# Kernel tuning notes

Hardware: AMD Instinct MI355X
Metric: run time of the kernel (lower is better)

The kernel has to match this reference:

```python
import jax, jax.numpy as jnp
import numpy as np

N_HEAD = 16
LORA_DIM = 16
LORA_ALPHA = 32


def setup_inputs() -> dict:
    key = jax.random.key(0)
    ks = jax.random.split(key, 8)
    B, S, D = 2, 2048, 1024
    std = 0.02
    return {
        "x": jax.random.normal(ks[0], (B, S, D), jnp.float32),
        "c_attn_w": jax.random.normal(ks[1], (D, 3 * D), jnp.float32) * std,
        "c_attn_b": jnp.zeros((3 * D,), jnp.float32),
        "c_proj_w": jax.random.normal(ks[2], (D, D), jnp.float32) * std,
        "c_proj_b": jnp.zeros((D,), jnp.float32),
        "q_a1": jax.random.normal(ks[3], (D, LORA_DIM), jnp.float32) * std,
        "q_a2": jax.random.normal(ks[4], (LORA_DIM, D), jnp.float32) * std,
        "v_a1": jax.random.normal(ks[5], (D, LORA_DIM), jnp.float32) * std,
        "v_a2": jax.random.normal(ks[6], (LORA_DIM, D), jnp.float32) * std,
    }


def reference(x, c_attn_w, c_attn_b, c_proj_w, c_proj_b, q_a1, q_a2, v_a1, v_a2):
    B, S, D = x.shape
    H = N_HEAD
    hd = D // H
    # NOTE: original code uses adapter_dim / adapter_alpha as the scale
    lora_scale = jnp.float32(LORA_DIM / LORA_ALPHA)

    qkv = x @ c_attn_w + c_attn_b                      # [B,S,3D]
    q, k, v = jnp.split(qkv, 3, axis=-1)
    q = q + ((x @ q_a1) @ q_a2) * lora_scale
    v = v + ((x @ v_a1) @ v_a2) * lora_scale

    def heads(t):
        return t.reshape(B, S, H, hd).transpose(0, 2, 1, 3)  # [B,H,S,hd]

    qh, kh, vh = heads(q), heads(k), heads(v)

    w = jnp.einsum('bhqd,bhkd->bhqk', qh, kh) / jnp.sqrt(jnp.float32(hd))
    bias = jnp.tril(jnp.ones((S, S), dtype=w.dtype))   # causal mask
    w = w * bias - jnp.float32(1e10) * (1 - bias)
    w = jax.nn.softmax(w, axis=-1)
    a = jnp.einsum('bhqk,bhkd->bhqd', w, vh)
    a = a.transpose(0, 2, 1, 3).reshape(B, S, D)       # merge heads
    a = a @ c_proj_w + c_proj_b

    present = jnp.stack((kh, vh))                      # [2,B,H,S,hd]
    return a, present
```

## Files before the change

kernel.cpp:

```cpp
#include <hip/hip_runtime.h>

#define T_TOK 4096
#define D_DIM 1024
#define N3    3072
#define S_LEN 2048
#define NH    16
#define HD    64
#define KAUG  1056

#define OUT_A_ELEMS   4194304
#define OUT_KV_ELEMS  4194304

typedef __attribute__((ext_vector_type(4))) float f32x4;
typedef __attribute__((ext_vector_type(16))) float f32x16;
typedef _Float16 f16x8 __attribute__((ext_vector_type(8)));
typedef _Float16 f16x4 __attribute__((ext_vector_type(4)));

union U4h { unsigned u[4]; f16x8 v; };

#define GHASH(r) ((((r) >> 1) ^ ((r) >> 3)) & 3)

__device__ __forceinline__ unsigned cvtpkh(float a, float b) {
    unsigned r;
    asm("v_cvt_pkrtz_f16_f32 %0, %1, %2" : "=v"(r) : "v"(a), "v"(b));
    return r;
}

#define GLL16(gp, lp) __builtin_amdgcn_global_load_lds( \
    (const __attribute__((address_space(1))) unsigned int*)(gp), \
    (__attribute__((address_space(3))) unsigned int*)(lp), 16, 0, 0)

#define MFMA16F(A, B, C) __builtin_amdgcn_mfma_f32_16x16x32_f16(A, B, C, 0, 0, 0)
#define MFMA32F(A, B, C) __builtin_amdgcn_mfma_f32_32x32x16_f16(A, B, C, 0, 0, 0)

__global__ __launch_bounds__(256) void lora1_v2(const float* __restrict__ x,
    const float* __restrict__ qa1, const float* __restrict__ va1,
    float* __restrict__ tq, float* __restrict__ tv) {
    int tid = threadIdx.x;
    int w = tid >> 6;
    int lane = tid & 63;
    int t = blockIdx.x * 4 + w;
    int cg = lane & 7;
    int ks = lane >> 3;
    const float* a1 = (cg < 4) ? qa1 : va1;
    int c4 = (cg & 3) * 4;
    const float* xr = x + (size_t)t * D_DIM + ks * 128;
    const float* ar = a1 + (size_t)(ks * 128) * 16 + c4;
    float4 acc = make_float4(0.f, 0.f, 0.f, 0.f);
#pragma unroll 8
    for (int j = 0; j < 128; ++j) {
        float xv = xr[j];
        float4 av = *(const float4*)&ar[j * 16];
        acc.x = fmaf(xv, av.x, acc.x);
        acc.y = fmaf(xv, av.y, acc.y);
        acc.z = fmaf(xv, av.z, acc.z);
        acc.w = fmaf(xv, av.w, acc.w);
    }
#pragma unroll
    for (int m = 8; m < 64; m <<= 1) {
        acc.x += __shfl_xor(acc.x, m);
        acc.y += __shfl_xor(acc.y, m);
        acc.z += __shfl_xor(acc.z, m);
        acc.w += __shfl_xor(acc.w, m);
    }
    if (lane < 8) {
        float* dst = (cg < 4) ? &tq[t * 16 + c4] : &tv[t * 16 + (cg - 4) * 4];
        *(float4*)dst = acc;
    }
}

__global__ __launch_bounds__(256) void splitA_f16(const float* __restrict__ x,
    const float* __restrict__ tq, const float* __restrict__ tv,
    _Float16* __restrict__ af) {
    int idx = blockIdx.x * 256 + threadIdx.x;
    const int total = T_TOK * (KAUG / 4);
    if (idx >= total) return;
    int t = idx / (KAUG / 4);
    int c4 = (idx - t * (KAUG / 4)) * 4;
    float4 v;
    if (c4 < D_DIM)           v = *(const float4*)&x[(size_t)t * D_DIM + c4];
    else if (c4 < D_DIM + 16) v = *(const float4*)&tq[t * 16 + (c4 - D_DIM)];
    else                      v = *(const float4*)&tv[t * 16 + (c4 - D_DIM - 16)];
    f16x4 h;
    h[0] = (_Float16)v.x; h[1] = (_Float16)v.y;
    h[2] = (_Float16)v.z; h[3] = (_Float16)v.w;
    *(f16x4*)&af[(size_t)t * KAUG + c4] = h;
}

__global__ __launch_bounds__(256) void splitW_f16(const float* __restrict__ w,
    const float* __restrict__ qa2, const float* __restrict__ va2,
    _Float16* __restrict__ bf) {
    __shared__ float T[32][65];
    int bn = blockIdx.x;
    int bk = blockIdx.y;
    int tid = threadIdx.x;
#pragma unroll
    for (int u = 0; u < 2; ++u) {
        int id = tid + 256 * u;
        int kr = id >> 4;
        int n4 = (id & 15) * 4;
        int k = bk * 32 + kr;
        int n = bn * 64 + n4;
        float4 v = make_float4(0.f, 0.f, 0.f, 0.f);
        if (k < D_DIM) {
            v = *(const float4*)&w[(size_t)k * N3 + n];
        } else if (k < D_DIM + 16) {
            if (n < D_DIM) {
                float4 q4 = *(const float4*)&qa2[(k - D_DIM) * D_DIM + n];
                v = make_float4(q4.x * 0.5f, q4.y * 0.5f, q4.z * 0.5f, q4.w * 0.5f);
            }
        } else {
            if (n >= 2 * D_DIM) {
                float4 q4 = *(const float4*)&va2[(k - D_DIM - 16) * D_DIM + (n - 2 * D_DIM)];
                v = make_float4(q4.x * 0.5f, q4.y * 0.5f, q4.z * 0.5f, q4.w * 0.5f);
            }
        }
        T[kr][n4 + 0] = v.x; T[kr][n4 + 1] = v.y;
        T[kr][n4 + 2] = v.z; T[kr][n4 + 3] = v.w;
    }
    __syncthreads();
    int n = tid >> 2;
    int k8 = (tid & 3) * 8;
    f16x8 hv;
#pragma unroll
    for (int j = 0; j < 8; ++j) hv[j] = (_Float16)T[k8 + j][n];
    int nr = bn * 64 + n;
    int gsw = (tid & 3) ^ GHASH(nr);
    size_t ro = (size_t)nr * KAUG + bk * 32 + gsw * 8;
    *(f16x8*)&bf[ro] = hv;
}

__global__ __launch_bounds__(256) void wprep_f16(const float* __restrict__ w,
    _Float16* __restrict__ bf) {
    __shared__ float T[32][65];
    int bn = blockIdx.x;
    int bk = blockIdx.y;
    int tid = threadIdx.x;
#pragma unroll
    for (int u = 0; u < 2; ++u) {
        int id = tid + 256 * u;
        int kr = id >> 4;
        int n4 = (id & 15) * 4;
        float4 v = *(const float4*)&w[(size_t)(bk * 32 + kr) * D_DIM + bn * 64 + n4];
        T[kr][n4 + 0] = v.x; T[kr][n4 + 1] = v.y;
        T[kr][n4 + 2] = v.z; T[kr][n4 + 3] = v.w;
    }
    __syncthreads();
    int n = tid >> 2;
    int k8 = (tid & 3) * 8;
    f16x8 hv;
#pragma unroll
    for (int j = 0; j < 8; ++j) hv[j] = (_Float16)T[k8 + j][n];
    int nr = bn * 64 + n;
    int gsw = (tid & 3) ^ GHASH(nr);
    size_t ro = (size_t)nr * D_DIM + bk * 32 + gsw * 8;
    *(f16x8*)&bf[ro] = hv;
}

__global__ __launch_bounds__(256, 3) void qkv_mfma(
    const _Float16* __restrict__ a_g, const _Float16* __restrict__ b_g,
    const float* __restrict__ bias, int mode,
    float* __restrict__ qstage, float* __restrict__ pres,
    _Float16* __restrict__ qf16, _Float16* __restrict__ kp,
    _Float16* __restrict__ vt) {
    __shared__ _Float16 Bf[2][2][128 * 32];
    int id = blockIdx.y * 24 + blockIdx.x;
    int nid = (id & 7) * 96 + (id >> 3);
    int bn = nid % 24;
    int bm = nid / 24;
    int tid = threadIdx.x;
    int w = tid >> 6, l = tid & 63;
    int wr = w >> 1, wc = w & 1;

    f32x4 acc[4][4];
#pragma unroll
    for (int i = 0; i < 4; ++i)
#pragma unroll
        for (int j = 0; j < 4; ++j)
            acc[i][j] = (f32x4){0.f, 0.f, 0.f, 0.f};

    int srow = l >> 2;
    int sk = (l & 3) * 8;
    const size_t b_base0 = (size_t)(bn * 128 + w * 32 + srow) * KAUG + sk;
    const size_t b_base1 = b_base0 + (size_t)16 * KAUG;
    const int ldso0 = (w * 32) * 32;
    const int ldso1 = (w * 32 + 16) * 32;

    int lrow = l & 15;
    int lg = l >> 4;

    const _Float16* aF[4];
#pragma unroll
    for (int i = 0; i < 4; ++i) {
        int row = bm * 128 + wr * 64 + i * 16 + lrow;
        aF[i] = a_g + (size_t)row * KAUG + lg * 8;
    }
    int roB[4];
#pragma unroll
    for (int j = 0; j < 4; ++j) {
        int Rb = wc * 64 + j * 16 + lrow;
        roB[j] = Rb * 32 + ((lg ^ GHASH(Rb)) * 8);
    }

    f16x8 cA0[4], cA1[4], nA0[4], nA1[4];

    GLL16(b_g + b_base0,      &Bf[0][0][ldso0]);
    GLL16(b_g + b_base1,      &Bf[0][0][ldso1]);
    GLL16(b_g + b_base0 + 32, &Bf[0][1][ldso0]);
    GLL16(b_g + b_base1 + 32, &Bf[0][1][ldso1]);
#pragma unroll
    for (int i = 0; i < 4; ++i) {
        cA0[i] = *(const f16x8*)(aF[i]);
        cA1[i] = *(const f16x8*)(aF[i] + 32);
    }
    asm volatile("s_waitcnt vmcnt(0)" ::: "memory");
    __builtin_amdgcn_s_barrier();

    for (int r = 0; r < 17; ++r) {
        int cur = r & 1;
        if (r < 16) {
            int kn = (r + 1) * 64;
            GLL16(b_g + b_base0 + kn, &Bf[cur ^ 1][0][ldso0]);
            GLL16(b_g + b_base1 + kn, &Bf[cur ^ 1][0][ldso1]);
            if (r < 15) {
                GLL16(b_g + b_base0 + kn + 32, &Bf[cur ^ 1][1][ldso0]);
                GLL16(b_g + b_base1 + kn + 32, &Bf[cur ^ 1][1][ldso1]);
            }
            __builtin_amdgcn_sched_barrier(0);
#pragma unroll
            for (int i = 0; i < 4; ++i) nA0[i] = *(const f16x8*)(aF[i] + kn);
            if (r < 15) {
#pragma unroll
                for (int i = 0; i < 4; ++i) nA1[i] = *(const f16x8*)(aF[i] + kn + 32);
            }
        }
        f16x8 fb[4];
#pragma unroll
        for (int j = 0; j < 4; ++j) fb[j] = *(const f16x8*)&Bf[cur][0][roB[j]];
#pragma unroll
        for (int i = 0; i < 4; ++i)
#pragma unroll
            for (int j = 0; j < 4; ++j)
                acc[i][j] = MFMA16F(cA0[i], fb[j], acc[i][j]);
        if (r < 16) {
#pragma unroll
            for (int j = 0; j < 4; ++j) fb[j] = *(const f16x8*)&Bf[cur][1][roB[j]];
#pragma unroll
            for (int i = 0; i < 4; ++i)
#pragma unroll
                for (int j = 0; j < 4; ++j)
                    acc[i][j] = MFMA16F(cA1[i], fb[j], acc[i][j]);
            if (r < 15) asm volatile("s_waitcnt vmcnt(8)" ::: "memory");
            else        asm volatile("s_waitcnt vmcnt(4)" ::: "memory");
            __builtin_amdgcn_s_barrier();
#pragma unroll
            for (int i = 0; i < 4; ++i) cA0[i] = nA0[i];
            if (r < 15) {
#pragma unroll
                for (int i = 0; i < 4; ++i) cA1[i] = nA1[i];
            }
        }
    }

    int seg = bn >> 3;
    int bb = bm >> 4;
#pragma unroll
    for (int j = 0; j < 4; ++j) {
        int n = bn * 128 + wc * 64 + j * 16 + lrow;
        float bz = bias[n];
        int h = (n >> 6) & 15;
        int d = n & 63;
        size_t rowbase = (size_t)(bb * NH + h) * S_LEN;
#pragma unroll
        for (int i = 0; i < 4; ++i) {
            int tb = bm * 128 + wr * 64 + i * 16 + (l >> 4) * 4;
            int s0 = tb & 2047;
            if (seg == 0) {
                if (mode == 0) {
#pragma unroll
                    for (int r = 0; r < 4; ++r)
                        qf16[(rowbase + s0 + r) * HD + d] =
                            (_Float16)((acc[i][j][r] + bz) * 0.125f);
                } else {
#pragma unroll
                    for (int r = 0; r < 4; ++r)
                        qstage[(rowbase + s0 + r) * HD + d] =
                            (acc[i][j][r] + bz) * 0.125f;
                }
            } else if (seg == 1) {
                int gsw = d >> 3;
#pragma unroll
                for (int r = 0; r < 4; ++r) {
                    float v = acc[i][j][r] + bz;
                    int s = s0 + r;
                    pres[(rowbase + s) * HD + d] = v;
                    if (mode == 0)
                        kp[(rowbase + s) * HD + ((gsw ^ (s & 7)) << 3) + (d & 7)] =
                            (_Float16)v;
                }
            } else {
                f16x4 pk;
#pragma unroll
                for (int r = 0; r < 4; ++r) {
                    float v = acc[i][j][r] + bz;
                    pres[OUT_KV_ELEMS + (rowbase + s0 + r) * HD + d] = v;
                    pk[r] = (_Float16)v;
                }
                if (mode == 0) {
                    int gp = ((s0 >> 3) & 7) ^ (d & 7);
                    *(f16x4*)&vt[((size_t)(bb * NH + h) * 64 + d) * 2048
                                 + (s0 & ~63) + (gp << 3) + (s0 & 7)] = pk;
                }
            }
        }
    }
}

__global__ __launch_bounds__(256, 3) void proj_mfma(
    const _Float16* __restrict__ a_g, const _Float16* __restrict__ b_g,
    const float* __restrict__ bias, float* __restrict__ outp) {
    __shared__ _Float16 Bf[2][2][128 * 32];
    int id = blockIdx.y * 8 + blockIdx.x;
    int nid = (id & 7) * 32 + (id >> 3);
    int bn = nid % 8;
    int bm = nid / 8;
    int tid = threadIdx.x;
    int w = tid >> 6, l = tid & 63;
    int wr = w >> 1, wc = w & 1;

    f32x4 acc[4][4];
#pragma unroll
    for (int i = 0; i < 4; ++i)
#pragma unroll
        for (int j = 0; j < 4; ++j)
            acc[i][j] = (f32x4){0.f, 0.f, 0.f, 0.f};

    int srow = l >> 2;
    int sk = (l & 3) * 8;
    const size_t b_base0 = (size_t)(bn * 128 + w * 32 + srow) * D_DIM + sk;
    const size_t b_base1 = b_base0 + (size_t)16 * D_DIM;
    const int ldso0 = (w * 32) * 32;
    const int ldso1 = (w * 32 + 16) * 32;

    int lrow = l & 15;
    int lg = l >> 4;

    const _Float16* aF[4];
#pragma unroll
    for (int i = 0; i < 4; ++i) {
        int row = bm * 128 + wr * 64 + i * 16 + lrow;
        aF[i] = a_g + (size_t)row * D_DIM + lg * 8;
    }
    int roB[4];
#pragma unroll
    for (int j = 0; j < 4; ++j) {
        int Rb = wc * 64 + j * 16 + lrow;
        roB[j] = Rb * 32 + ((lg ^ GHASH(Rb)) * 8);
    }

    f16x8 cA0[4], cA1[4], nA0[4], nA1[4];

    GLL16(b_g + b_base0,      &Bf[0][0][ldso0]);
    GLL16(b_g + b_base1,      &Bf[0][0][ldso1]);
    GLL16(b_g + b_base0 + 32, &Bf[0][1][ldso0]);
    GLL16(b_g + b_base1 + 32, &Bf[0][1][ldso1]);
#pragma unroll
    for (int i = 0; i < 4; ++i) {
        cA0[i] = *(const f16x8*)(aF[i]);
        cA1[i] = *(const f16x8*)(aF[i] + 32);
    }
    asm volatile("s_waitcnt vmcnt(0)" ::: "memory");
    __builtin_amdgcn_s_barrier();

    for (int r = 0; r < 16; ++r) {
        int cur = r & 1;
        if (r < 15) {
            int kn = (r + 1) * 64;
            GLL16(b_g + b_base0 + kn,      &Bf[cur ^ 1][0][ldso0]);
            GLL16(b_g + b_base1 + kn,      &Bf[cur ^ 1][0][ldso1]);
            GLL16(b_g + b_base0 + kn + 32, &Bf[cur ^ 1][1][ldso0]);
            GLL16(b_g + b_base1 + kn + 32, &Bf[cur ^ 1][1][ldso1]);
            __builtin_amdgcn_sched_barrier(0);
#pragma unroll
            for (int i = 0; i < 4; ++i) {
                nA0[i] = *(const f16x8*)(aF[i] + kn);
                nA1[i] = *(const f16x8*)(aF[i] + kn + 32);
            }
        }
        f16x8 fb[4];
#pragma unroll
        for (int j = 0; j < 4; ++j) fb[j] = *(const f16x8*)&Bf[cur][0][roB[j]];
#pragma unroll
        for (int i = 0; i < 4; ++i)
#pragma unroll
            for (int j = 0; j < 4; ++j)
                acc[i][j] = MFMA16F(cA0[i], fb[j], acc[i][j]);
#pragma unroll
        for (int j = 0; j < 4; ++j) fb[j] = *(const f16x8*)&Bf[cur][1][roB[j]];
#pragma unroll
        for (int i = 0; i < 4; ++i)
#pragma unroll
            for (int j = 0; j < 4; ++j)
                acc[i][j] = MFMA16F(cA1[i], fb[j], acc[i][j]);
        if (r < 15) {
            asm volatile("s_waitcnt vmcnt(8)" ::: "memory");
            __builtin_amdgcn_s_barrier();
#pragma unroll
            for (int i = 0; i < 4; ++i) { cA0[i] = nA0[i]; cA1[i] = nA1[i]; }
        }
    }

#pragma unroll
    for (int j = 0; j < 4; ++j) {
        int n = bn * 128 + wc * 64 + j * 16 + lrow;
        float bz = bias[n];
#pragma unroll
        for (int i = 0; i < 4; ++i) {
            int tbase = bm * 128 + wr * 64 + i * 16 + (l >> 4) * 4;
#pragma unroll
            for (int r = 0; r < 4; ++r)
                outp[(size_t)(tbase + r) * D_DIM + n] = acc[i][j][r] + bz;
        }
    }
}

__device__ __forceinline__ void stage_tile(
    const _Float16* __restrict__ kp, const _Float16* __restrict__ vt,
    _Float16 (*ldsb)[4096], int w, int l, int bh, int kv0) {
    if (w < 2) {
        const _Float16* gp = kp
            + ((size_t)bh * 2048 + kv0 + w * 32 + (l >> 3)) * 64 + (l & 7) * 8;
        _Float16* lp = ldsb[0] + (w * 32) * 64;
#pragma unroll
        for (int i = 0; i < 4; ++i)
            GLL16(gp + i * 512, lp + i * 512);
    } else {
        int wv = w - 2;
        const _Float16* gp = vt
            + ((size_t)bh * 64 + wv * 32 + (l >> 3)) * 2048 + kv0 + (l & 7) * 8;
        _Float16* lp = ldsb[1] + (wv * 32) * 64;
#pragma unroll
        for (int i = 0; i < 4; ++i)
            GLL16(gp + (size_t)i * 8 * 2048, lp + i * 512);
    }
}

#define QROW(r) ((((r) & 3) + 8 * ((r) >> 2)) + 4 * g)

__global__ __launch_bounds__(256, 4) void attn_mfma(
    const _Float16* __restrict__ q_h,
    const _Float16* __restrict__ kp, const _Float16* __restrict__ vt,
    _Float16* __restrict__ aout) {
    __shared__ __align__(16) _Float16 lds[2][2][4096];
    int bh = blockIdx.x;
    int qi = (int)gridDim.y - 1 - blockIdx.y;
    int tid = threadIdx.x;
    int w = tid >> 6, l = tid & 63;
    int qloc = l & 31, g = l >> 5;
    int q0 = qi * 128;
    int qg = q0 + w * 32 + qloc;

    f16x8 qf[4];
    {
        const _Float16* qrow = q_h + ((size_t)bh * S_LEN + qg) * HD;
#pragma unroll
        for (int t = 0; t < 4; ++t)
            qf[t] = *(const f16x8*)&qrow[t * 16 + g * 8];
    }

    f32x16 o0, o1;
#pragma unroll
    for (int r = 0; r < 16; ++r) { o0[r] = 0.f; o1[r] = 0.f; }
    float m_run = -1e30f, l_run = 0.f;

    int nt = 2 * qi + 2;
    int qwmax = q0 + w * 32 + 31;

    stage_tile(kp, vt, lds[0], w, l, bh, 0);
    __syncthreads();

    for (int t = 0; t < nt; ++t) {
        int kv0 = t * 64;
        int bi = t & 1;
        if (t + 1 < nt)
            stage_tile(kp, vt, lds[bi ^ 1], w, l, bh, (t + 1) * 64);

        if (kv0 <= qwmax) {
            const _Float16* Kp = lds[bi][0];
            const _Float16* Vp = lds[bi][1];

            f32x16 s0, s1;
#pragma unroll
            for (int r = 0; r < 16; ++r) { s0[r] = 0.f; s1[r] = 0.f; }

            __builtin_amdgcn_s_setprio(1);
#pragma unroll
            for (int tt = 0; tt < 4; ++tt) {
                int gr = ((2 * tt + g) ^ (qloc & 7)) * 8;
                f16x8 a0 = *(const f16x8*)&Kp[qloc * 64 + gr];
                f16x8 a1 = *(const f16x8*)&Kp[(32 + qloc) * 64 + gr];
                s0 = MFMA32F(a0, qf[tt], s0);
                s1 = MFMA32F(a1, qf[tt], s1);
            }
            __builtin_amdgcn_s_setprio(0);

            if (kv0 + 63 > q0 + w * 32) {
#pragma unroll
                for (int r = 0; r < 16; ++r) {
                    int kk = kv0 + QROW(r);
                    if (kk > qg)      s0[r] = -1e30f;
                    if (kk + 32 > qg) s1[r] = -1e30f;
                }
            }

            float mx = s0[0];
#pragma unroll
            for (int r = 1; r < 16; ++r) mx = fmaxf(mx, s0[r]);
#pragma unroll
            for (int r = 0; r < 16; ++r) mx = fmaxf(mx, s1[r]);
            mx = fmaxf(mx, __shfl_xor(mx, 32));
            float mnew = fmaxf(m_run, mx);
            float al = __expf(m_run - mnew);
            m_run = mnew;
            float rs = 0.f;
#pragma unroll
            for (int r = 0; r < 16; ++r) { s0[r] = __expf(s0[r] - mnew); rs += s0[r]; }
#pragma unroll
            for (int r = 0; r < 16; ++r) { s1[r] = __expf(s1[r] - mnew); rs += s1[r]; }
            rs += __shfl_xor(rs, 32);
            l_run = l_run * al + rs;
#pragma unroll
            for (int r = 0; r < 16; ++r) {
                float ar = __shfl(al, QROW(r));
                o0[r] *= ar; o1[r] *= ar;
            }

            __builtin_amdgcn_s_setprio(1);
#pragma unroll
            for (int ks = 0; ks < 4; ++ks) {
                const int b = (ks & 1) * 8;
                unsigned w0, w1, w2, w3;
                if (ks < 2) {
                    w0 = cvtpkh(s0[b + 0], s0[b + 1]);
                    w1 = cvtpkh(s0[b + 2], s0[b + 3]);
                    w2 = cvtpkh(s0[b + 4], s0[b + 5]);
                    w3 = cvtpkh(s0[b + 6], s0[b + 7]);
                } else {
                    w0 = cvtpkh(s1[b + 0], s1[b + 1]);
                    w1 = cvtpkh(s1[b + 2], s1[b + 3]);
                    w2 = cvtpkh(s1[b + 4], s1[b + 5]);
                    w3 = cvtpkh(s1[b + 6], s1[b + 7]);
                }
                asm("v_permlane32_swap_b32 %0, %1" : "+v"(w0), "+v"(w2));
                asm("v_permlane32_swap_b32 %0, %1" : "+v"(w1), "+v"(w3));
                U4h u; u.u[0] = w0; u.u[1] = w1; u.u[2] = w2; u.u[3] = w3;
                f16x8 pa = u.v;
                int gr = ((2 * ks + g) ^ (qloc & 7)) * 8;
                f16x8 v0 = *(const f16x8*)&Vp[qloc * 64 + gr];
                f16x8 v1 = *(const f16x8*)&Vp[(32 + qloc) * 64 + gr];
                o0 = MFMA32F(pa, v0, o0);
                o1 = MFMA32F(pa, v1, o1);
            }
            __builtin_amdgcn_s_setprio(0);
        }
        __syncthreads();
    }

    int bb = bh >> 4, h = bh & 15;
#pragma unroll
    for (int r = 0; r < 16; ++r) {
        float li = __shfl(l_run, QROW(r));
        float inv = 1.f / li;
        int qq = q0 + w * 32 + QROW(r);
        size_t base = ((size_t)(bb * S_LEN + qq)) * D_DIM + h * HD + qloc;
        aout[base]      = (_Float16)(o0[r] * inv);
        aout[base + 32] = (_Float16)(o1[r] * inv);
    }
}

#define LSTR 68
__global__ __launch_bounds__(256) void attn_kernel(const float* __restrict__ q_s,
    const float* __restrict__ k_s, const float* __restrict__ v_s,
    float* __restrict__ a_s) {
    __shared__ float Qt[64][LSTR];
    __shared__ float KP[64][LSTR];
    __shared__ float Vs[64][LSTR];
    int bh = blockIdx.x;
    int qi = 31 - blockIdx.y;
    int tid = threadIdx.x;
    int tx = tid & 15, ty = tid >> 4;

#pragma unroll
    for (int qq = 0; qq < 4; ++qq) {
        int q  = qq * 16 + (tid >> 4);
        int d4 = (tid & 15) * 4;
        float4 v = *(const float4*)&q_s[((size_t)bh * S_LEN + qi * 64 + q) * HD + d4];
        Qt[d4 + 0][q] = v.x; Qt[d4 + 1][q] = v.y;
        Qt[d4 + 2][q] = v.z; Qt[d4 + 3][q] = v.w;
    }

    float o[4][4];
#pragma unroll
    for (int r = 0; r < 4; ++r)
#pragma unroll
        for (int c = 0; c < 4; ++c) o[r][c] = 0.f;
    float mrow[4] = {-1e30f, -1e30f, -1e30f, -1e30f};
    float lrow[4] = {0.f, 0.f, 0.f, 0.f};

    for (int kt = 0; kt <= qi; ++kt) {
        __syncthreads();
#pragma unroll
        for (int kk2 = 0; kk2 < 4; ++kk2) {
            int k  = kk2 * 16 + (tid >> 4);
            int d4 = (tid & 15) * 4;
            size_t rowoff = ((size_t)bh * S_LEN + kt * 64 + k) * HD + d4;
            float4 kv4 = *(const float4*)&k_s[rowoff];
            KP[d4 + 0][k] = kv4.x; KP[d4 + 1][k] = kv4.y;
            KP[d4 + 2][k] = kv4.z; KP[d4 + 3][k] = kv4.w;
            float4 vv4 = *(const float4*)&v_s[rowoff];
            *(float4*)&Vs[k][d4] = vv4;
        }
        __syncthreads();

        float s[4][4];
#pragma unroll
        for (int r = 0; r < 4; ++r)
#pragma unroll
            for (int c = 0; c < 4; ++c) s[r][c] = 0.f;
#pragma unroll 8
        for (int d = 0; d < 64; ++d) {
            float4 qv = *(const float4*)&Qt[d][ty * 4];
            float4 kv = *(const float4*)&KP[d][tx * 4];
            float qa[4] = {qv.x, qv.y, qv.z, qv.w};
            float ka[4] = {kv.x, kv.y, kv.z, kv.w};
#pragma unroll
            for (int r = 0; r < 4; ++r)
#pragma unroll
                for (int c = 0; c < 4; ++c)
                    s[r][c] = fmaf(qa[r], ka[c], s[r][c]);
        }
        if (kt == qi) {
#pragma unroll
            for (int r = 0; r < 4; ++r)
#pragma unroll
                for (int c = 0; c < 4; ++c)
                    if (tx * 4 + c > ty * 4 + r) s[r][c] = -1e30f;
        }
        __syncthreads();

        float p[4][4];
#pragma unroll
        for (int r = 0; r < 4; ++r) {
            float mx = fmaxf(fmaxf(s[r][0], s[r][1]), fmaxf(s[r][2], s[r][3]));
            mx = fmaxf(mx, __shfl_xor(mx, 1));
            mx = fmaxf(mx, __shfl_xor(mx, 2));
            mx = fmaxf(mx, __shfl_xor(mx, 4));
            mx = fmaxf(mx, __shfl_xor(mx, 8));
            float mn = fmaxf(mrow[r], mx);
            float alpha = __expf(mrow[r] - mn);
            mrow[r] = mn;
            float rsum = 0.f;
#pragma unroll
            for (int c = 0; c < 4; ++c) {
                p[r][c] = __expf(s[r][c] - mn);
                rsum += p[r][c];
            }
            rsum += __shfl_xor(rsum, 1);
            rsum += __shfl_xor(rsum, 2);
            rsum += __shfl_xor(rsum, 4);
            rsum += __shfl_xor(rsum, 8);
            lrow[r] = lrow[r] * alpha + rsum;
#pragma unroll
            for (int c = 0; c < 4; ++c) o[r][c] *= alpha;
            *(float4*)&KP[ty * 4 + r][tx * 4] =
                make_float4(p[r][0], p[r][1], p[r][2], p[r][3]);
        }
        __syncthreads();

#pragma unroll 8
        for (int k = 0; k < 64; ++k) {
            float4 vv = *(const float4*)&Vs[k][tx * 4];
            float va[4] = {vv.x, vv.y, vv.z, vv.w};
#pragma unroll
            for (int r = 0; r < 4; ++r) {
                float pr = KP[ty * 4 + r][k];
#pragma unroll
                for (int c = 0; c < 4; ++c)
                    o[r][c] = fmaf(pr, va[c], o[r][c]);
            }
        }
    }

    int b = bh >> 4, h = bh & 15;
#pragma unroll
    for (int r = 0; r < 4; ++r) {
        int i = qi * 64 + ty * 4 + r;
        float inv = 1.f / lrow[r];
        *(float4*)&a_s[((size_t)(b * S_LEN + i)) * D_DIM + h * HD + tx * 4] =
            make_float4(o[r][0] * inv, o[r][1] * inv, o[r][2] * inv, o[r][3] * inv);
    }
}

__global__ __launch_bounds__(256) void proj_kernel(const float* __restrict__ A,
    const float* __restrict__ w, const float* __restrict__ bias,
    float* __restrict__ outp) {
    __shared__ float As[128][17];
    __shared__ float Bs[16][64];
    int bx = blockIdx.x;
    int by = blockIdx.y;
    int tid = threadIdx.x;
    int tx = tid & 15, ty = tid >> 4;

    float c[8][4];
#pragma unroll
    for (int i = 0; i < 8; ++i)
#pragma unroll
        for (int j = 0; j < 4; ++j) c[i][j] = 0.f;

    for (int k0 = 0; k0 < D_DIM; k0 += 16) {
#pragma unroll
        for (int u = 0; u < 2; ++u) {
            int f4 = tid + 256 * u;
            int row = f4 >> 2;
            int kk4 = (f4 & 3) * 4;
            float4 av = *(const float4*)&A[(size_t)(by * 128 + row) * D_DIM + k0 + kk4];
            As[row][kk4 + 0] = av.x; As[row][kk4 + 1] = av.y;
            As[row][kk4 + 2] = av.z; As[row][kk4 + 3] = av.w;
        }
        {
            int kkb = tid >> 4;
            int col4 = (tid & 15) * 4;
            *(float4*)&Bs[kkb][col4] =
                *(const float4*)&w[(size_t)(k0 + kkb) * D_DIM + bx * 64 + col4];
        }
        __syncthreads();
#pragma unroll
        for (int kk = 0; kk < 16; ++kk) {
            float4 bv = *(const float4*)&Bs[kk][tx * 4];
#pragma unroll
            for (int i = 0; i < 8; ++i) {
                float a = As[ty * 8 + i][kk];
                c[i][0] = fmaf(a, bv.x, c[i][0]);
                c[i][1] = fmaf(a, bv.y, c[i][1]);
                c[i][2] = fmaf(a, bv.z, c[i][2]);
                c[i][3] = fmaf(a, bv.w, c[i][3]);
            }
        }
        __syncthreads();
    }

    int ncol = bx * 64 + tx * 4;
    float4 bias4 = *(const float4*)&bias[ncol];
#pragma unroll
    for (int i = 0; i < 8; ++i) {
        int t = by * 128 + ty * 8 + i;
        *(float4*)&outp[(size_t)t * D_DIM + ncol] =
            make_float4(c[i][0] + bias4.x, c[i][1] + bias4.y,
                        c[i][2] + bias4.z, c[i][3] + bias4.w);
    }
}

extern "C" void kernel_launch(void* const* d_in, const int* in_sizes, int n_in,
                              void* d_out, int out_size, void* d_ws, size_t ws_size,
                              hipStream_t stream) {
    const float* x        = (const float*)d_in[0];
    const float* c_attn_w = (const float*)d_in[1];
    const float* c_attn_b = (const float*)d_in[2];
    const float* c_proj_w = (const float*)d_in[3];
    const float* c_proj_b = (const float*)d_in[4];
    const float* q_a1     = (const float*)d_in[5];
    const float* q_a2     = (const float*)d_in[6];
    const float* v_a1     = (const float*)d_in[7];
    const float* v_a2     = (const float*)d_in[8];

    float* outf   = (float*)d_out;
    float* qstage = outf;
    float* pres   = outf + OUT_A_ELEMS;

    char* wsb = (char*)d_ws;
    float* tq = (float*)wsb;
    float* tv = (float*)(wsb + 262144);
    _Float16* w_f16  = (_Float16*)(wsb + 524288);
    _Float16* a_f16  = (_Float16*)(wsb + 7012352);
    _Float16* kp_f16 = (_Float16*)(wsb + 16777216);
    _Float16* vt_f16 = (_Float16*)(wsb + 25165824);
    _Float16* q_h16  = (_Float16*)(wsb + 33554432);
    _Float16* aout_f16 = (_Float16*)wsb;
    _Float16* wp_f16   = (_Float16*)(wsb + 8388608);
    const size_t WS_FULL = 41943040;
    const size_t WS_MID  = 16777216;

    lora1_v2<<<dim3(1024), dim3(256), 0, stream>>>(x, q_a1, v_a1, tq, tv);

    if (ws_size >= WS_FULL) {
        splitA_f16<<<dim3((T_TOK * (KAUG / 4) + 255) / 256), dim3(256), 0, stream>>>(
            x, tq, tv, a_f16);
        splitW_f16<<<dim3(48, KAUG / 32), dim3(256), 0, stream>>>(
            c_attn_w, q_a2, v_a2, w_f16);
        qkv_mfma<<<dim3(24, 32), dim3(256), 0, stream>>>(
            a_f16, w_f16, c_attn_b, 0, nullptr, pres, q_h16, kp_f16, vt_f16);
        attn_mfma<<<dim3(32, 16), dim3(256), 0, stream>>>(
            q_h16, kp_f16, vt_f16, aout_f16);
        wprep_f16<<<dim3(16, 32), dim3(256), 0, stream>>>(c_proj_w, wp_f16);
        proj_mfma<<<dim3(8, 32), dim3(256), 0, stream>>>(
            aout_f16, wp_f16, c_proj_b, outf);
    } else if (ws_size >= WS_MID) {
        float* a_s = (float*)wsb;
        splitA_f16<<<dim3((T_TOK * (KAUG / 4) + 255) / 256), dim3(256), 0, stream>>>(
            x, tq, tv, a_f16);
        splitW_f16<<<dim3(48, KAUG / 32), dim3(256), 0, stream>>>(
            c_attn_w, q_a2, v_a2, w_f16);
        qkv_mfma<<<dim3(24, 32), dim3(256), 0, stream>>>(
            a_f16, w_f16, c_attn_b, 1, qstage, pres, nullptr, nullptr, nullptr);
        attn_kernel<<<dim3(32, 32), dim3(256), 0, stream>>>(
            qstage, pres, pres + OUT_KV_ELEMS, a_s);
        proj_kernel<<<dim3(16, 32), dim3(256), 0, stream>>>(
            a_s, c_proj_w, c_proj_b, outf);
    } else {
        float* a_s2 = tv + 65536;
        attn_kernel<<<dim3(32, 32), dim3(256), 0, stream>>>(
            qstage, pres, pres + OUT_KV_ELEMS, a_s2);
        proj_kernel<<<dim3(16, 32), dim3(256), 0, stream>>>(
            a_s2, c_proj_w, c_proj_b, outf);
    }
}
```

Measured before the change: 250.8 us.

## Replace LDS double-buffered B staging with direct global register loads in GEMMs

The QKV and projection GEMM kernels no longer stage the weight tile through LDS with async global-to-LDS copies, double buffering and barriers. Each wave now loads both A and B fragments straight from global memory into registers in a simple unrolled k-loop. The weight prep kernels drop the XOR swizzle because LDS bank conflicts no longer apply. This removes barrier and LDS overhead but loses the explicit prefetch overlap and the sharing of B tiles across waves, so B reuse now depends on cache.

Measured after the change: 277.7 us. +10.7%, slower.

```diff
diff --git a/kernel.cpp b/kernel.cpp
--- a/kernel.cpp
+++ b/kernel.cpp
@@ -17,8 +17,6 @@
 typedef _Float16 f16x4 __attribute__((ext_vector_type(4)));
 
 union U4h { unsigned u[4]; f16x8 v; };
-
-#define GHASH(r) ((((r) >> 1) ^ ((r) >> 3)) & 3)
 
 __device__ __forceinline__ unsigned cvtpkh(float a, float b) {
     unsigned r;
@@ -124,9 +122,7 @@
     f16x8 hv;
 #pragma unroll
     for (int j = 0; j < 8; ++j) hv[j] = (_Float16)T[k8 + j][n];
-    int nr = bn * 64 + n;
-    int gsw = (tid & 3) ^ GHASH(nr);
-    size_t ro = (size_t)nr * KAUG + bk * 32 + gsw * 8;
+    size_t ro = (size_t)(bn * 64 + n) * KAUG + bk * 32 + k8;
     *(f16x8*)&bf[ro] = hv;
 }
 
@@ -151,9 +147,7 @@
     f16x8 hv;
 #pragma unroll
     for (int j = 0; j < 8; ++j) hv[j] = (_Float16)T[k8 + j][n];
-    int nr = bn * 64 + n;
-    int gsw = (tid & 3) ^ GHASH(nr);
-    size_t ro = (size_t)nr * D_DIM + bk * 32 + gsw * 8;
+    size_t ro = (size_t)(bn * 64 + n) * D_DIM + bk * 32 + k8;
     *(f16x8*)&bf[ro] = hv;
 }
 
@@ -163,7 +157,6 @@
     float* __restrict__ qstage, float* __restrict__ pres,
     _Float16* __restrict__ qf16, _Float16* __restrict__ kp,
     _Float16* __restrict__ vt) {
-    __shared__ _Float16 Bf[2][2][128 * 32];
     int id = blockIdx.y * 24 + blockIdx.x;
     int nid = (id & 7) * 96 + (id >> 3);
     int bn = nid % 24;
@@ -171,6 +164,8 @@
     int tid = threadIdx.x;
     int w = tid >> 6, l = tid & 63;
     int wr = w >> 1, wc = w & 1;
+    int lrow = l & 15;
+    int lg = l >> 4;
 
     f32x4 acc[4][4];
 #pragma unroll
@@ -179,87 +174,31 @@
         for (int j = 0; j < 4; ++j)
             acc[i][j] = (f32x4){0.f, 0.f, 0.f, 0.f};
 
-    int srow = l >> 2;
-    int sk = (l & 3) * 8;
-    const size_t b_base0 = (size_t)(bn * 128 + w * 32 + srow) * KAUG + sk;
-    const size_t b_base1 = b_base0 + (size_t)16 * KAUG;
-    const int ldso0 = (w * 32) * 32;
-    const int ldso1 = (w * 32 + 16) * 32;
-
-    int lrow = l & 15;
-    int lg = l >> 4;
-
     const _Float16* aF[4];
+    const _Float16* bF[4];
 #pragma unroll
     for (int i = 0; i < 4; ++i) {
         int row = bm * 128 + wr * 64 + i * 16 + lrow;
         aF[i] = a_g + (size_t)row * KAUG + lg * 8;
     }
-    int roB[4];
 #pragma unroll
     for (int j = 0; j < 4; ++j) {
-        int Rb = wc * 64 + j * 16 + lrow;
-        roB[j] = Rb * 32 + ((lg ^ GHASH(Rb)) * 8);
-    }
-
-    f16x8 cA0[4], cA1[4], nA0[4], nA1[4];
-
-    GLL16(b_g + b_base0,      &Bf[0][0][ldso0]);
-    GLL16(b_g + b_base1,      &Bf[0][0][ldso1]);
-    GLL16(b_g + b_base0 + 32, &Bf[0][1][ldso0]);
-    GLL16(b_g + b_base1 + 32, &Bf[0][1][ldso1]);
-#pragma unroll
-    for (int i = 0; i < 4; ++i) {
-        cA0[i] = *(const f16x8*)(aF[i]);
-        cA1[i] = *(const f16x8*)(aF[i] + 32);
-    }
-    asm volatile("s_waitcnt vmcnt(0)" ::: "memory");
-    __builtin_amdgcn_s_barrier();
-
-    for (int r = 0; r < 17; ++r) {
-        int cur = r & 1;
-        if (r < 16) {
-            int kn = (r + 1) * 64;
-            GLL16(b_g + b_base0 + kn, &Bf[cur ^ 1][0][ldso0]);
-            GLL16(b_g + b_base1 + kn, &Bf[cur ^ 1][0][ldso1]);
-            if (r < 15) {
-                GLL16(b_g + b_base0 + kn + 32, &Bf[cur ^ 1][1][ldso0]);
-                GLL16(b_g + b_base1 + kn + 32, &Bf[cur ^ 1][1][ldso1]);
-            }
-            __builtin_amdgcn_sched_barrier(0);
-#pragma unroll
-            for (int i = 0; i < 4; ++i) nA0[i] = *(const f16x8*)(aF[i] + kn);
-            if (r < 15) {
-#pragma unroll
-                for (int i = 0; i < 4; ++i) nA1[i] = *(const f16x8*)(aF[i] + kn + 32);
-            }
-        }
-        f16x8 fb[4];
-#pragma unroll
-        for (int j = 0; j < 4; ++j) fb[j] = *(const f16x8*)&Bf[cur][0][roB[j]];
+        int nr = bn * 128 + wc * 64 + j * 16 + lrow;
+        bF[j] = b_g + (size_t)nr * KAUG + lg * 8;
+    }
+
+#pragma unroll 3
+    for (int k0 = 0; k0 < KAUG; k0 += 32) {
+        f16x8 fa[4], fb[4];
+#pragma unroll
+        for (int i = 0; i < 4; ++i) fa[i] = *(const f16x8*)(aF[i] + k0);
+#pragma unroll
+        for (int j = 0; j < 4; ++j) fb[j] = *(const f16x8*)(bF[j] + k0);
 #pragma unroll
         for (int i = 0; i < 4; ++i)
 #pragma unroll
             for (int j = 0; j < 4; ++j)
-                acc[i][j] = MFMA16F(cA0[i], fb[j], acc[i][j]);
-        if (r < 16) {
-#pragma unroll
-            for (int j = 0; j < 4; ++j) fb[j] = *(const f16x8*)&Bf[cur][1][roB[j]];
-#pragma unroll
-            for (int i = 0; i < 4; ++i)
-#pragma unroll
-                for (int j = 0; j < 4; ++j)
-                    acc[i][j] = MFMA16F(cA1[i], fb[j], acc[i][j]);
-            if (r < 15) asm volatile("s_waitcnt vmcnt(8)" ::: "memory");
-            else        asm volatile("s_waitcnt vmcnt(4)" ::: "memory");
-            __builtin_amdgcn_s_barrier();
-#pragma unroll
-            for (int i = 0; i < 4; ++i) cA0[i] = nA0[i];
-            if (r < 15) {
-#pragma unroll
-                for (int i = 0; i < 4; ++i) cA1[i] = nA1[i];
-            }
-        }
+                acc[i][j] = MFMA16F(fa[i], fb[j], acc[i][j]);
     }
 
     int seg = bn >> 3;
@@ -319,7 +258,6 @@
 __global__ __launch_bounds__(256, 3) void proj_mfma(
     const _Float16* __restrict__ a_g, const _Float16* __restrict__ b_g,
     const float* __restrict__ bias, float* __restrict__ outp) {
-    __shared__ _Float16 Bf[2][2][128 * 32];
     int id = blockIdx.y * 8 + blockIdx.x;
     int nid = (id & 7) * 32 + (id >> 3);
     int bn = nid % 8;
@@ -327,6 +265,8 @@
     int tid = threadIdx.x;
     int w = tid >> 6, l = tid & 63;
     int wr = w >> 1, wc = w & 1;
+    int lrow = l & 15;
+    int lg = l >> 4;
 
     f32x4 acc[4][4];
 #pragma unroll
@@ -335,79 +275,31 @@
         for (int j = 0; j < 4; ++j)
             acc[i][j] = (f32x4){0.f, 0.f, 0.f, 0.f};
 
-    int srow = l >> 2;
-    int sk = (l & 3) * 8;
-    const size_t b_base0 = (size_t)(bn * 128 + w * 32 + srow) * D_DIM + sk;
-    const size_t b_base1 = b_base0 + (size_t)16 * D_DIM;
-    const int ldso0 = (w * 32) * 32;
-    const int ldso1 = (w * 32 + 16) * 32;
-
-    int lrow = l & 15;
-    int lg = l >> 4;
-
     const _Float16* aF[4];
+    const _Float16* bF[4];
 #pragma unroll
     for (int i = 0; i < 4; ++i) {
         int row = bm * 128 + wr * 64 + i * 16 + lrow;
         aF[i] = a_g + (size_t)row * D_DIM + lg * 8;
     }
-    int roB[4];
 #pragma unroll
     for (int j = 0; j < 4; ++j) {
-        int Rb = wc * 64 + j * 16 + lrow;
-        roB[j] = Rb * 32 + ((lg ^ GHASH(Rb)) * 8);
-    }
-
-    f16x8 cA0[4], cA1[4], nA0[4], nA1[4];
-
-    GLL16(b_g + b_base0,      &Bf[0][0][ldso0]);
-    GLL16(b_g + b_base1,      &Bf[0][0][ldso1]);
-    GLL16(b_g + b_base0 + 32, &Bf[0][1][ldso0]);
-    GLL16(b_g + b_base1 + 32, &Bf[0][1][ldso1]);
-#pragma unroll
-    for (int i = 0; i < 4; ++i) {
-        cA0[i] = *(const f16x8*)(aF[i]);
-        cA1[i] = *(const f16x8*)(aF[i] + 32);
-    }
-    asm volatile("s_waitcnt vmcnt(0)" ::: "memory");
-    __builtin_amdgcn_s_barrier();
-
-    for (int r = 0; r < 16; ++r) {
-        int cur = r & 1;
-        if (r < 15) {
-            int kn = (r + 1) * 64;
-            GLL16(b_g + b_base0 + kn,      &Bf[cur ^ 1][0][ldso0]);
-            GLL16(b_g + b_base1 + kn,      &Bf[cur ^ 1][0][ldso1]);
-            GLL16(b_g + b_base0 + kn + 32, &Bf[cur ^ 1][1][ldso0]);
-            GLL16(b_g + b_base1 + kn + 32, &Bf[cur ^ 1][1][ldso1]);
-            __builtin_amdgcn_sched_barrier(0);
-#pragma unroll
-            for (int i = 0; i < 4; ++i) {
-                nA0[i] = *(const f16x8*)(aF[i] + kn);
-                nA1[i] = *(const f16x8*)(aF[i] + kn + 32);
-            }
-        }
-        f16x8 fb[4];
-#pragma unroll
-        for (int j = 0; j < 4; ++j) fb[j] = *(const f16x8*)&Bf[cur][0][roB[j]];
+        int nr = bn * 128 + wc * 64 + j * 16 + lrow;
+        bF[j] = b_g + (size_t)nr * D_DIM + lg * 8;
+    }
+
+#pragma unroll 4
+    for (int k0 = 0; k0 < D_DIM; k0 += 32) {
+        f16x8 fa[4], fb[4];
+#pragma unroll
+        for (int i = 0; i < 4; ++i) fa[i] = *(const f16x8*)(aF[i] + k0);
+#pragma unroll
+        for (int j = 0; j < 4; ++j) fb[j] = *(const f16x8*)(bF[j] + k0);
 #pragma unroll
         for (int i = 0; i < 4; ++i)
 #pragma unroll
             for (int j = 0; j < 4; ++j)
-                acc[i][j] = MFMA16F(cA0[i], fb[j], acc[i][j]);
-#pragma unroll
-        for (int j = 0; j < 4; ++j) fb[j] = *(const f16x8*)&Bf[cur][1][roB[j]];
-#pragma unroll
-        for (int i = 0; i < 4; ++i)
-#pragma unroll
-            for (int j = 0; j < 4; ++j)
-                acc[i][j] = MFMA16F(cA1[i], fb[j], acc[i][j]);
-        if (r < 15) {
-            asm volatile("s_waitcnt vmcnt(8)" ::: "memory");
-            __builtin_amdgcn_s_barrier();
-#pragma unroll
-            for (int i = 0; i < 4; ++i) { cA0[i] = nA0[i]; cA1[i] = nA1[i]; }
-        }
+                acc[i][j] = MFMA16F(fa[i], fb[j], acc[i][j]);
     }
 
 #pragma unroll
```
